# Performance work log

Measured on AMD Instinct MI355X. Metric: run time of the kernel, lower is better.

The kernel has to match this reference:

```python
import jax, jax.numpy as jnp
from jax import lax
import numpy as np
import math

ORDER = 5            # bessel_order
CUTOFF = 25e9        # cutoff_hz
FS = 100e9           # sampling rate
B, T = 64, 131072    # batch, time samples


def _bessel_ba(order, cutoff, fs):
    """numpy re-implementation of scipy.signal.bessel(order, cutoff, fs=fs, norm='mag')."""
    n = order
    # reverse Bessel polynomial theta_n(s), highest power first (monic)
    c = np.array([math.factorial(2 * n - k) / (2.0 ** (n - k) * math.factorial(k) * math.factorial(n - k))
                  for k in range(n, -1, -1)])
    p = np.roots(c)            # analog prototype poles
    a0 = c[-1]                 # DC gain numerator (H(s) = a0 / theta(s))
    # 'mag' norm: find w3 with |H(jw3)| = 1/sqrt(2)  <=>  |theta(jw3)|^2 = 2*a0^2
    f = lambda w: np.abs(np.polyval(c, 1j * w)) ** 2 - 2.0 * a0 ** 2
    lo, hi = 0.0, 1.0
    while f(hi) < 0.0:
        hi *= 2.0
    for _ in range(200):
        mid = 0.5 * (lo + hi)
        if f(mid) < 0.0:
            lo = mid
        else:
            hi = mid
    w3 = 0.5 * (lo + hi)
    p = p / w3
    k = a0 / w3 ** n
    # prewarp + lowpass-to-lowpass
    warped = 2.0 * fs * np.tan(np.pi * cutoff / fs)
    p = p * warped
    k = k * warped ** n
    # bilinear transform (zeros of analog prototype: none -> n zeros at z=-1)
    fs2 = 2.0 * fs
    pz = (fs2 + p) / (fs2 - p)
    kz = k / np.real(np.prod(fs2 - p))
    b = kz * np.real(np.poly(-np.ones(n)))
    a = np.real(np.poly(pz))
    return b, a


def setup_inputs() -> dict:
    key = jax.random.key(0)
    x = jax.random.normal(key, (B, T), dtype=jnp.float32)
    b, a = _bessel_ba(ORDER, CUTOFF, FS)
    return {"x": x,
            "b": jnp.asarray(b, jnp.float32),
            "a": jnp.asarray(a, jnp.float32)}


def _lfilter(x, a, b):
    """Direct-form I IIR filter along last axis; x: (B, T), a/b: (N+1,)."""
    a0 = a[0]
    bn = b / a0
    an = a / a0
    nb = bn.shape[0]
    # FIR part f[t] = sum_j b[j] * x[t-j] via causal convolution
    f = lax.conv_general_dilated(
        x[:, None, :], jnp.flip(bn)[None, None, :],
        window_strides=(1,), padding=[(nb - 1, 0)],
        dimension_numbers=("NCH", "OIH", "NCH"))[:, 0, :]          # (B, T)
    ar = an[1:]                   # (N,) feedback taps a[1..N]
    N = ar.shape[0]
    def step(carry, f_t):         # carry: (B, N) = [y[t-1], ..., y[t-N]]
        y_t = f_t - carry @ ar    # (B,)
        carry = jnp.concatenate([y_t[:, None], carry[:, :-1]], axis=1)
        return carry, y_t
    _, y = lax.scan(step, jnp.zeros((x.shape[0], N), x.dtype), f.T)
    return y.T                    # (B, T)


def reference(x, b, a):
    xmax = jnp.max(jnp.abs(x))
    return xmax * _lfilter(x / xmax, a, b)
```

## Files before the change

### kernel.cpp

```cpp
#include <hip/hip_runtime.h>


constexpr int T_LEN  = 131072;
constexpr int B_ROWS = 64;
constexpr int CHUNK  = 32;
constexpr int WARM   = 64;
constexpr int HEAD   = 96;
constexpr int BLOCK  = 256;
constexpr int SPAN   = BLOCK * CHUNK;
constexpr int BPR    = T_LEN / SPAN;
constexpr int XTOT   = HEAD + SPAN;
constexpr int XPAD   = XTOT + XTOT / 32;
constexpr int YPAD   = SPAN + SPAN / 32;

__device__ __forceinline__ int padi(int s) { return s + (s >> 5); }

__global__ __launch_bounds__(BLOCK, 2) void bessel_tile_kernel(
    const float* __restrict__ x,
    const float* __restrict__ bco,
    const float* __restrict__ aco,
    float* __restrict__ y)
{
    __shared__ float xs[XPAD];
    __shared__ float ys[YPAD];

    const int b    = blockIdx.x;
    const int row  = b / BPR;
    const int tile = b % BPR;
    const int base = tile * SPAN;
    const int j    = threadIdx.x;

    const float* __restrict__ xr = x + (size_t)row * T_LEN;
    float* __restrict__       yr = y + (size_t)row * T_LEN;

    if (tile == 0) {
        for (int s = j; s < HEAD; s += BLOCK)
            xs[padi(s)] = 0.0f;
        #pragma unroll
        for (int it = 0; it < SPAN / 4 / BLOCK; ++it) {
            int k = j + it * BLOCK;
            float4 v = *(const float4*)(xr + base + 4 * k);
            int S = HEAD + 4 * k;
            int p = padi(S);
            xs[p] = v.x; xs[p + 1] = v.y; xs[p + 2] = v.z; xs[p + 3] = v.w;
        }
    } else {
        for (int k = j; k < XTOT / 4; k += BLOCK) {
            float4 v = *(const float4*)(xr + base - HEAD + 4 * k);
            int S = 4 * k;
            int p = padi(S);
            xs[p] = v.x; xs[p + 1] = v.y; xs[p + 2] = v.z; xs[p + 3] = v.w;
        }
    }

    const float inv = 1.0f / aco[0];
    const float b0 = bco[0] * inv, b1 = bco[1] * inv, b2 = bco[2] * inv,
                b3 = bco[3] * inv, b4 = bco[4] * inv, b5 = bco[5] * inv;
    const float a1 = aco[1] * inv, a2 = aco[2] * inv, a3 = aco[3] * inv,
                a4 = aco[4] * inv, a5 = aco[5] * inv;

    __syncthreads();

    {
        const int S0 = HEAD + j * CHUNK;
        const int ws = S0 - WARM;
        float y1 = 0.f, y2 = 0.f, y3 = 0.f, y4 = 0.f, y5 = 0.f;
        float xm1 = xs[padi(ws - 1)], xm2 = xs[padi(ws - 2)], xm3 = xs[padi(ws - 3)],
              xm4 = xs[padi(ws - 4)], xm5 = xs[padi(ws - 5)];

        #pragma unroll 8
        for (int t = ws; t < S0; ++t) {
            float xv = xs[padi(t)];
            float f = b0 * xv + b1 * xm1 + b2 * xm2 + b3 * xm3 + b4 * xm4 + b5 * xm5;
            float o = f - a1 * y1 - a2 * y2 - a3 * y3 - a4 * y4 - a5 * y5;
            y5 = y4; y4 = y3; y3 = y2; y2 = y1; y1 = o;
            xm5 = xm4; xm4 = xm3; xm3 = xm2; xm2 = xm1; xm1 = xv;
        }
        #pragma unroll 8
        for (int t = S0; t < S0 + CHUNK; ++t) {
            float xv = xs[padi(t)];
            float f = b0 * xv + b1 * xm1 + b2 * xm2 + b3 * xm3 + b4 * xm4 + b5 * xm5;
            float o = f - a1 * y1 - a2 * y2 - a3 * y3 - a4 * y4 - a5 * y5;
            y5 = y4; y4 = y3; y3 = y2; y2 = y1; y1 = o;
            xm5 = xm4; xm4 = xm3; xm3 = xm2; xm2 = xm1; xm1 = xv;
            ys[padi(t - HEAD)] = o;
        }
    }

    __syncthreads();

    #pragma unroll
    for (int it = 0; it < SPAN / 4 / BLOCK; ++it) {
        int S = 4 * (j + it * BLOCK);
        int p = padi(S);
        float4 v;
        v.x = ys[p]; v.y = ys[p + 1]; v.z = ys[p + 2]; v.w = ys[p + 3];
        *(float4*)(yr + base + S) = v;
    }
}

extern "C" void kernel_launch(void* const* d_in, const int* in_sizes, int n_in,
                              void* d_out, int out_size, void* d_ws, size_t ws_size,
                              hipStream_t stream) {
    const float* x   = (const float*)d_in[0];
    const float* bco = (const float*)d_in[1];
    const float* aco = (const float*)d_in[2];
    float* y = (float*)d_out;

    const int grid = B_ROWS * BPR;
    bessel_tile_kernel<<<grid, BLOCK, 0, stream>>>(x, bco, aco, y);
}
```

Measured before the change: 97.92 us.

## Halve warmup, drop output LDS staging, write float4 directly per thread

Shortens the per-chunk IIR warmup from 64 to 32 samples and shrinks the input halo to match, cutting redundant recurrence work. Removes the output shared-memory buffer and the second barrier, so each thread writes its own 32 outputs straight to global memory as float4 stores. Raises the launch-bounds occupancy hint to 4 blocks. The shorter warmup increases truncation error from the zero initial state, and the per-thread strided stores are less coalesced than the old staged writes.

```diff
diff --git a/kernel.cpp b/kernel.cpp
--- a/kernel.cpp
+++ b/kernel.cpp
@@ -4,25 +4,23 @@
 constexpr int T_LEN  = 131072;
 constexpr int B_ROWS = 64;
 constexpr int CHUNK  = 32;
-constexpr int WARM   = 64;
-constexpr int HEAD   = 96;
+constexpr int WARM   = 32;
+constexpr int HEAD   = 64;
 constexpr int BLOCK  = 256;
 constexpr int SPAN   = BLOCK * CHUNK;
 constexpr int BPR    = T_LEN / SPAN;
 constexpr int XTOT   = HEAD + SPAN;
 constexpr int XPAD   = XTOT + XTOT / 32;
-constexpr int YPAD   = SPAN + SPAN / 32;
 
 __device__ __forceinline__ int padi(int s) { return s + (s >> 5); }
 
-__global__ __launch_bounds__(BLOCK, 2) void bessel_tile_kernel(
+__global__ __launch_bounds__(BLOCK, 4) void bessel_tile_kernel(
     const float* __restrict__ x,
     const float* __restrict__ bco,
     const float* __restrict__ aco,
     float* __restrict__ y)
 {
     __shared__ float xs[XPAD];
-    __shared__ float ys[YPAD];
 
     const int b    = blockIdx.x;
     const int row  = b / BPR;
@@ -30,25 +28,22 @@
     const int base = tile * SPAN;
     const int j    = threadIdx.x;
 
-    const float* __restrict__ xr = x + (size_t)row * T_LEN;
-    float* __restrict__       yr = y + (size_t)row * T_LEN;
+    const float* __restrict__ xr  = x + (size_t)row * T_LEN;
+    float* __restrict__       yrp = y + (size_t)row * T_LEN + base;
 
     if (tile == 0) {
-        for (int s = j; s < HEAD; s += BLOCK)
-            xs[padi(s)] = 0.0f;
+        if (j < HEAD) xs[padi(j)] = 0.0f;
         #pragma unroll
         for (int it = 0; it < SPAN / 4 / BLOCK; ++it) {
             int k = j + it * BLOCK;
             float4 v = *(const float4*)(xr + base + 4 * k);
-            int S = HEAD + 4 * k;
-            int p = padi(S);
+            int p = padi(HEAD + 4 * k);
             xs[p] = v.x; xs[p + 1] = v.y; xs[p + 2] = v.z; xs[p + 3] = v.w;
         }
     } else {
         for (int k = j; k < XTOT / 4; k += BLOCK) {
             float4 v = *(const float4*)(xr + base - HEAD + 4 * k);
-            int S = 4 * k;
-            int p = padi(S);
+            int p = padi(4 * k);
             xs[p] = v.x; xs[p + 1] = v.y; xs[p + 2] = v.z; xs[p + 3] = v.w;
         }
     }
@@ -61,41 +56,36 @@
 
     __syncthreads();
 
-    {
-        const int S0 = HEAD + j * CHUNK;
-        const int ws = S0 - WARM;
-        float y1 = 0.f, y2 = 0.f, y3 = 0.f, y4 = 0.f, y5 = 0.f;
-        float xm1 = xs[padi(ws - 1)], xm2 = xs[padi(ws - 2)], xm3 = xs[padi(ws - 3)],
-              xm4 = xs[padi(ws - 4)], xm5 = xs[padi(ws - 5)];
+    const int S0 = HEAD + j * CHUNK;
+    int t = S0 - WARM;
 
-        #pragma unroll 8
-        for (int t = ws; t < S0; ++t) {
+    float y1 = 0.f, y2 = 0.f, y3 = 0.f, y4 = 0.f, y5 = 0.f;
+    float xm1 = xs[padi(t - 1)], xm2 = xs[padi(t - 2)], xm3 = xs[padi(t - 3)],
+          xm4 = xs[padi(t - 4)], xm5 = xs[padi(t - 5)];
+
+    #pragma unroll
+    for (int i = 0; i < WARM; ++i, ++t) {
+        float xv = xs[padi(t)];
+        float f = b0 * xv + b1 * xm1 + b2 * xm2 + b3 * xm3 + b4 * xm4 + b5 * xm5;
+        float o = f - a1 * y1 - a2 * y2 - a3 * y3 - a4 * y4 - a5 * y5;
+        y5 = y4; y4 = y3; y3 = y2; y2 = y1; y1 = o;
+        xm5 = xm4; xm4 = xm3; xm3 = xm2; xm2 = xm1; xm1 = xv;
+    }
+
+    float* outp = yrp + j * CHUNK;
+    #pragma unroll
+    for (int g = 0; g < CHUNK / 4; ++g) {
+        float4 ov;
+        #pragma unroll
+        for (int i = 0; i < 4; ++i, ++t) {
             float xv = xs[padi(t)];
             float f = b0 * xv + b1 * xm1 + b2 * xm2 + b3 * xm3 + b4 * xm4 + b5 * xm5;
             float o = f - a1 * y1 - a2 * y2 - a3 * y3 - a4 * y4 - a5 * y5;
             y5 = y4; y4 = y3; y3 = y2; y2 = y1; y1 = o;
             xm5 = xm4; xm4 = xm3; xm3 = xm2; xm2 = xm1; xm1 = xv;
+            (&ov.x)[i] = o;
         }
-        #pragma unroll 8
-        for (int t = S0; t < S0 + CHUNK; ++t) {
-            float xv = xs[padi(t)];
-            float f = b0 * xv + b1 * xm1 + b2 * xm2 + b3 * xm3 + b4 * xm4 + b5 * xm5;
-            float o = f - a1 * y1 - a2 * y2 - a3 * y3 - a4 * y4 - a5 * y5;
-            y5 = y4; y4 = y3; y3 = y2; y2 = y1; y1 = o;
-            xm5 = xm4; xm4 = xm3; xm3 = xm2; xm2 = xm1; xm1 = xv;
-            ys[padi(t - HEAD)] = o;
-        }
-    }
-
-    __syncthreads();
-
-    #pragma unroll
-    for (int it = 0; it < SPAN / 4 / BLOCK; ++it) {
-        int S = 4 * (j + it * BLOCK);
-        int p = padi(S);
-        float4 v;
-        v.x = ys[p]; v.y = ys[p + 1]; v.z = ys[p + 2]; v.w = ys[p + 3];
-        *(float4*)(yr + base + S) = v;
+        *(float4*)(outp + 4 * g) = ov;
     }
 }
 
```

After: 93.00 us. -5.0%, faster.
